# Performance work log

Measured on AMD Instinct MI355X. Metric: run time of the kernel, lower is better.

The kernel has to match this reference:

```python
import jax, jax.numpy as jnp
import numpy as np


def _dct2_basis(N, K):
    # Unnormalized DCT-II basis as used by torch_dct.dct(norm=None):
    #   X_k = 2 * sum_n x_n * cos(pi * (2n+1) * k / (2N))
    # Returns [K, N]: only the first K (low-frequency) rows are needed.
    n = jnp.arange(N, dtype=jnp.float32)
    k = jnp.arange(K, dtype=jnp.float32)
    return 2.0 * jnp.cos(jnp.pi * (2.0 * n[None, :] + 1.0) * k[:, None] / (2.0 * N))


def setup_inputs() -> dict:
    key = jax.random.key(0)
    x = jax.random.normal(key, (16, 64, 256, 256), dtype=jnp.float32)
    return {"x": x, "num_coeffs": 32}


def reference(x, num_coeffs):
    # x: [B, C, H, W]. Equivalent to dct.dct_2d(x)[:, :, :K, :K] (norm=None),
    # computed directly via truncated cosine-basis GEMMs.
    B, C, H, W = x.shape
    Ch = _dct2_basis(H, num_coeffs)  # [K, H]
    Cw = _dct2_basis(W, num_coeffs)  # [K, W]
    # [B, C, K, K] = Ch @ x @ Cw^T over the last two dims
    return jnp.einsum('kh,bchw,lw->bckl', Ch, x, Cw)
```

## Files before the change

### kernel.cpp

```cpp
#include <hip/hip_runtime.h>
#include <math.h>
#include <string.h>

#define KC 32

typedef __attribute__((ext_vector_type(8))) short bf16x8;
typedef __attribute__((ext_vector_type(4))) float f32x4;

__device__ __forceinline__ unsigned pack2_bf16(float a, float b) {
    unsigned ua = __float_as_uint(a); ua += 0x7fffu + ((ua >> 16) & 1u);
    unsigned ub = __float_as_uint(b); ub += 0x7fffu + ((ub >> 16) & 1u);
    return (ua >> 16) | (ub & 0xffff0000u);
}

static unsigned short h_tab[8192];
static const bool h_tab_ready = []() {
    for (int t = 0; t < 1024; ++t) {
        int c = t >> 7, sub = (t >> 6) & 1, lane = t & 63;
        int g = lane >> 4, cl = lane & 15;
        for (int i = 0; i < 8; ++i) {
            int A = 32 * c + 8 * g + i;
            int B = sub * 16 + cl;
            double v = 2.0 * cos(M_PI * (double)(2 * A + 1) * (double)B / 512.0);
            float f = (float)v;
            unsigned u;
            memcpy(&u, &f, 4);
            u += 0x7fffu + ((u >> 16) & 1u);
            h_tab[t * 8 + i] = (unsigned short)(u >> 16);
        }
    }
    return true;
}();

__global__ __launch_bounds__(256, 4) void dct_trunc_kernel(
    const float* __restrict__ x, float* __restrict__ out,
    const unsigned short* __restrict__ tab) {
    __shared__ uint4 ldsbuf[2560];
    char* lds = (char*)ldsbuf;
    const bf16x8* __restrict__ tabv = (const bf16x8*)tab;

    const int tid  = threadIdx.x;
    const int lane = tid & 63;
    const int wv   = tid >> 6;
    const int g    = lane >> 4;
    const int cl   = lane & 15;
    const int img  = blockIdx.x;
    const float* __restrict__ xi = x + (size_t)img * 65536;

    const int srow = tid >> 3;
    const int sc   = tid & 7;

    float4 pf0, pf1, pf2, pf3, pf4, pf5, pf6, pf7;

#define STAGE_LOAD(c_) do { \
    const float* s_ = xi + (size_t)(c_) * 32 + (size_t)srow * 256 + sc * 4; \
    pf0 = *(const float4*)(s_ + 0 * 8192); \
    pf1 = *(const float4*)(s_ + 1 * 8192); \
    pf2 = *(const float4*)(s_ + 2 * 8192); \
    pf3 = *(const float4*)(s_ + 3 * 8192); \
    pf4 = *(const float4*)(s_ + 4 * 8192); \
    pf5 = *(const float4*)(s_ + 5 * 8192); \
    pf6 = *(const float4*)(s_ + 6 * 8192); \
    pf7 = *(const float4*)(s_ + 7 * 8192); \
} while (0)

#define STAGE_WRITE(base_) do { \
    char* b_ = lds + (base_) + srow * 80 + sc * 8; \
    *(uint2*)(b_ + 0 * 2560) = make_uint2(pack2_bf16(pf0.x, pf0.y), pack2_bf16(pf0.z, pf0.w)); \
    *(uint2*)(b_ + 1 * 2560) = make_uint2(pack2_bf16(pf1.x, pf1.y), pack2_bf16(pf1.z, pf1.w)); \
    *(uint2*)(b_ + 2 * 2560) = make_uint2(pack2_bf16(pf2.x, pf2.y), pack2_bf16(pf2.z, pf2.w)); \
    *(uint2*)(b_ + 3 * 2560) = make_uint2(pack2_bf16(pf3.x, pf3.y), pack2_bf16(pf3.z, pf3.w)); \
    *(uint2*)(b_ + 4 * 2560) = make_uint2(pack2_bf16(pf4.x, pf4.y), pack2_bf16(pf4.z, pf4.w)); \
    *(uint2*)(b_ + 5 * 2560) = make_uint2(pack2_bf16(pf5.x, pf5.y), pack2_bf16(pf5.z, pf5.w)); \
    *(uint2*)(b_ + 6 * 2560) = make_uint2(pack2_bf16(pf6.x, pf6.y), pack2_bf16(pf6.z, pf6.w)); \
    *(uint2*)(b_ + 7 * 2560) = make_uint2(pack2_bf16(pf7.x, pf7.y), pack2_bf16(pf7.z, pf7.w)); \
} while (0)

    f32x4 a00 = {0.f,0.f,0.f,0.f}, a01 = a00, a10 = a00, a11 = a00;
    f32x4 a20 = a00, a21 = a00, a30 = a00, a31 = a00;

    STAGE_LOAD(0);
    STAGE_WRITE(0);

    const int frow = cl * 80 + g * 16;

    #pragma unroll 2
    for (int c = 0; c < 8; ++c) {
        __syncthreads();

        bf16x8 bf0 = tabv[(c * 2 + 0) * 64 + lane];
        bf16x8 bf1 = tabv[(c * 2 + 1) * 64 + lane];
        if (c < 7) STAGE_LOAD(c + 1);

        const char* xb = lds + (c & 1) * 20480;
        bf16x8 xf0 = *(const bf16x8*)(xb + (wv +  0) * 1280 + frow);
        bf16x8 xf1 = *(const bf16x8*)(xb + (wv +  4) * 1280 + frow);
        bf16x8 xf2 = *(const bf16x8*)(xb + (wv +  8) * 1280 + frow);
        bf16x8 xf3 = *(const bf16x8*)(xb + (wv + 12) * 1280 + frow);

        a00 = __builtin_amdgcn_mfma_f32_16x16x32_bf16(xf0, bf0, a00, 0, 0, 0);
        a01 = __builtin_amdgcn_mfma_f32_16x16x32_bf16(xf0, bf1, a01, 0, 0, 0);
        a10 = __builtin_amdgcn_mfma_f32_16x16x32_bf16(xf1, bf0, a10, 0, 0, 0);
        a11 = __builtin_amdgcn_mfma_f32_16x16x32_bf16(xf1, bf1, a11, 0, 0, 0);
        a20 = __builtin_amdgcn_mfma_f32_16x16x32_bf16(xf2, bf0, a20, 0, 0, 0);
        a21 = __builtin_amdgcn_mfma_f32_16x16x32_bf16(xf2, bf1, a21, 0, 0, 0);
        a30 = __builtin_amdgcn_mfma_f32_16x16x32_bf16(xf3, bf0, a30, 0, 0, 0);
        a31 = __builtin_amdgcn_mfma_f32_16x16x32_bf16(xf3, bf1, a31, 0, 0, 0);

        if (c < 7) STAGE_WRITE(((c + 1) & 1) * 20480);
    }

#define UTW(q_, A0_, A1_) do { \
    char* u0 = lds + (0 * 16 + cl) * 528 + (wv + 4 * (q_)) * 32 + g * 8; \
    char* u1 = lds + (1 * 16 + cl) * 528 + (wv + 4 * (q_)) * 32 + g * 8; \
    *(uint2*)u0 = make_uint2(pack2_bf16(A0_[0], A0_[1]), pack2_bf16(A0_[2], A0_[3])); \
    *(uint2*)u1 = make_uint2(pack2_bf16(A1_[0], A1_[1]), pack2_bf16(A1_[2], A1_[3])); \
} while (0)
    UTW(0, a00, a01);
    UTW(1, a10, a11);
    UTW(2, a20, a21);
    UTW(3, a30, a31);
    __syncthreads();

    const int mt2 = wv >> 1;
    const int nt2 = wv & 1;
    f32x4 acc2 = {0.f, 0.f, 0.f, 0.f};
    const char* ub = lds + (nt2 * 16 + cl) * 528 + g * 16;
    #pragma unroll
    for (int c2 = 0; c2 < 8; ++c2) {
        bf16x8 af = tabv[(c2 * 2 + mt2) * 64 + lane];
        bf16x8 uf = *(const bf16x8*)(ub + c2 * 64);
        acc2 = __builtin_amdgcn_mfma_f32_16x16x32_bf16(af, uf, acc2, 0, 0, 0);
    }

    float* op = out + (size_t)img * 1024 + (mt2 * 16 + g * 4) * 32 + nt2 * 16 + cl;
    op[0]  = acc2[0];
    op[32] = acc2[1];
    op[64] = acc2[2];
    op[96] = acc2[3];
}

extern "C" void kernel_launch(void* const* d_in, const int* in_sizes, int n_in,
                              void* d_out, int out_size, void* d_ws, size_t ws_size,
                              hipStream_t stream) {
    const float* x = (const float*)d_in[0];
    float* out = (float*)d_out;
    unsigned short* tab = (unsigned short*)d_ws;

    (void)h_tab_ready;
    hipMemcpyAsync(tab, h_tab, sizeof(h_tab), hipMemcpyHostToDevice, stream);

    const int n_imgs = in_sizes[0] / 65536;
    dct_trunc_kernel<<<n_imgs, 256, 0, stream>>>(x, out, tab);
}
```

Baseline: 50.50 us.

## Load MFMA A-fragments directly from global memory, dropping LDS staging

```diff
diff --git a/kernel.cpp b/kernel.cpp
--- a/kernel.cpp
+++ b/kernel.cpp
@@ -11,6 +11,17 @@
     unsigned ua = __float_as_uint(a); ua += 0x7fffu + ((ua >> 16) & 1u);
     unsigned ub = __float_as_uint(b); ub += 0x7fffu + ((ub >> 16) & 1u);
     return (ua >> 16) | (ub & 0xffff0000u);
+}
+
+__device__ __forceinline__ bf16x8 pack8(const float* __restrict__ p) {
+    float4 u = *(const float4*)p;
+    float4 v = *(const float4*)(p + 4);
+    union { unsigned w[4]; bf16x8 v8; } r;
+    r.w[0] = pack2_bf16(u.x, u.y);
+    r.w[1] = pack2_bf16(u.z, u.w);
+    r.w[2] = pack2_bf16(v.x, v.y);
+    r.w[3] = pack2_bf16(v.z, v.w);
+    return r.v8;
 }
 
 static unsigned short h_tab[8192];
@@ -35,7 +46,7 @@
 __global__ __launch_bounds__(256, 4) void dct_trunc_kernel(
     const float* __restrict__ x, float* __restrict__ out,
     const unsigned short* __restrict__ tab) {
-    __shared__ uint4 ldsbuf[2560];
+    __shared__ uint4 ldsbuf[1056];
     char* lds = (char*)ldsbuf;
     const bf16x8* __restrict__ tabv = (const bf16x8*)tab;
 
@@ -47,56 +58,20 @@
     const int img  = blockIdx.x;
     const float* __restrict__ xi = x + (size_t)img * 65536;
 
-    const int srow = tid >> 3;
-    const int sc   = tid & 7;
-
-    float4 pf0, pf1, pf2, pf3, pf4, pf5, pf6, pf7;
-
-#define STAGE_LOAD(c_) do { \
-    const float* s_ = xi + (size_t)(c_) * 32 + (size_t)srow * 256 + sc * 4; \
-    pf0 = *(const float4*)(s_ + 0 * 8192); \
-    pf1 = *(const float4*)(s_ + 1 * 8192); \
-    pf2 = *(const float4*)(s_ + 2 * 8192); \
-    pf3 = *(const float4*)(s_ + 3 * 8192); \
-    pf4 = *(const float4*)(s_ + 4 * 8192); \
-    pf5 = *(const float4*)(s_ + 5 * 8192); \
-    pf6 = *(const float4*)(s_ + 6 * 8192); \
-    pf7 = *(const float4*)(s_ + 7 * 8192); \
-} while (0)
-
-#define STAGE_WRITE(base_) do { \
-    char* b_ = lds + (base_) + srow * 80 + sc * 8; \
-    *(uint2*)(b_ + 0 * 2560) = make_uint2(pack2_bf16(pf0.x, pf0.y), pack2_bf16(pf0.z, pf0.w)); \
-    *(uint2*)(b_ + 1 * 2560) = make_uint2(pack2_bf16(pf1.x, pf1.y), pack2_bf16(pf1.z, pf1.w)); \
-    *(uint2*)(b_ + 2 * 2560) = make_uint2(pack2_bf16(pf2.x, pf2.y), pack2_bf16(pf2.z, pf2.w)); \
-    *(uint2*)(b_ + 3 * 2560) = make_uint2(pack2_bf16(pf3.x, pf3.y), pack2_bf16(pf3.z, pf3.w)); \
-    *(uint2*)(b_ + 4 * 2560) = make_uint2(pack2_bf16(pf4.x, pf4.y), pack2_bf16(pf4.z, pf4.w)); \
-    *(uint2*)(b_ + 5 * 2560) = make_uint2(pack2_bf16(pf5.x, pf5.y), pack2_bf16(pf5.z, pf5.w)); \
-    *(uint2*)(b_ + 6 * 2560) = make_uint2(pack2_bf16(pf6.x, pf6.y), pack2_bf16(pf6.z, pf6.w)); \
-    *(uint2*)(b_ + 7 * 2560) = make_uint2(pack2_bf16(pf7.x, pf7.y), pack2_bf16(pf7.z, pf7.w)); \
-} while (0)
-
     f32x4 a00 = {0.f,0.f,0.f,0.f}, a01 = a00, a10 = a00, a11 = a00;
     f32x4 a20 = a00, a21 = a00, a30 = a00, a31 = a00;
 
-    STAGE_LOAD(0);
-    STAGE_WRITE(0);
+    const float* __restrict__ xb = xi + (size_t)(wv * 16 + cl) * 256 + 8 * g;
 
-    const int frow = cl * 80 + g * 16;
-
-    #pragma unroll 2
+    #pragma unroll
     for (int c = 0; c < 8; ++c) {
-        __syncthreads();
-
         bf16x8 bf0 = tabv[(c * 2 + 0) * 64 + lane];
         bf16x8 bf1 = tabv[(c * 2 + 1) * 64 + lane];
-        if (c < 7) STAGE_LOAD(c + 1);
 
-        const char* xb = lds + (c & 1) * 20480;
-        bf16x8 xf0 = *(const bf16x8*)(xb + (wv +  0) * 1280 + frow);
-        bf16x8 xf1 = *(const bf16x8*)(xb + (wv +  4) * 1280 + frow);
-        bf16x8 xf2 = *(const bf16x8*)(xb + (wv +  8) * 1280 + frow);
-        bf16x8 xf3 = *(const bf16x8*)(xb + (wv + 12) * 1280 + frow);
+        bf16x8 xf0 = pack8(xb + 32 * c +  0 * 16384);
+        bf16x8 xf1 = pack8(xb + 32 * c +  1 * 16384);
+        bf16x8 xf2 = pack8(xb + 32 * c +  2 * 16384);
+        bf16x8 xf3 = pack8(xb + 32 * c +  3 * 16384);
 
         a00 = __builtin_amdgcn_mfma_f32_16x16x32_bf16(xf0, bf0, a00, 0, 0, 0);
         a01 = __builtin_amdgcn_mfma_f32_16x16x32_bf16(xf0, bf1, a01, 0, 0, 0);
@@ -106,8 +81,6 @@
         a21 = __builtin_amdgcn_mfma_f32_16x16x32_bf16(xf2, bf1, a21, 0, 0, 0);
         a30 = __builtin_amdgcn_mfma_f32_16x16x32_bf16(xf3, bf0, a30, 0, 0, 0);
         a31 = __builtin_amdgcn_mfma_f32_16x16x32_bf16(xf3, bf1, a31, 0, 0, 0);
-
-        if (c < 7) STAGE_WRITE(((c + 1) & 1) * 20480);
     }
 
 #define UTW(q_, A0_, A1_) do { \
```

Result: slower. 63.90 us (+26.5%).
